# Kernel optimization log

Hardware: AMD Instinct MI355X
Metric: run time of the kernel (lower is better)

The kernel has to match this reference:

```python
import jax, jax.numpy as jnp
import numpy as np

N_NODES = 50000
N_EDGES = 800000
N_GRAPHS = 500
D_IN, D_HID, D_OUT = 128, 128, 64


def setup_inputs() -> dict:
    key = jax.random.key(0)
    ks = jax.random.split(key, 8)
    n_feat = jax.random.normal(ks[0], (N_NODES, D_IN), jnp.float32)
    src = jax.random.randint(ks[1], (N_EDGES,), 0, N_NODES, jnp.int32)
    dst = jax.random.randint(ks[2], (N_EDGES,), 0, N_NODES, jnp.int32)
    graph_ids = jnp.sort(jax.random.randint(ks[3], (N_NODES,), 0, N_GRAPHS, jnp.int32))
    W0 = jax.random.normal(ks[4], (D_IN, D_HID), jnp.float32) * 0.05
    b0 = jnp.zeros((D_HID,), jnp.float32)
    W1 = jax.random.normal(ks[5], (D_HID, D_HID), jnp.float32) * 0.05
    b1 = jnp.zeros((D_HID,), jnp.float32)
    W2 = jax.random.normal(ks[6], (D_HID, D_OUT), jnp.float32) * 0.05
    b2 = jnp.zeros((D_OUT,), jnp.float32)
    return dict(n_feat=n_feat, W0=W0, b0=b0, W1=W1, b1=b1, W2=W2, b2=b2,
                src=src, dst=dst, graph_ids=graph_ids)


def _gcn_layer(h, W, b, src, dst, norm_out, norm_in):
    # DGL GraphConv, norm='both': D_out^{-1/2} gather, sum-aggregate at dst,
    # D_in^{-1/2}, then linear transform + bias.
    m = (h * norm_out[:, None])[src]                        # [E, d] gather
    agg = jax.ops.segment_sum(m, dst, num_segments=N_NODES)  # [N, d] scatter-add
    return (agg * norm_in[:, None]) @ W + b


def reference(n_feat, W0, b0, W1, b1, W2, b2, src, dst, graph_ids):
    ones_e = jnp.ones((N_EDGES,), jnp.float32)
    deg_out = jax.ops.segment_sum(ones_e, src, num_segments=N_NODES)
    deg_in = jax.ops.segment_sum(ones_e, dst, num_segments=N_NODES)
    norm_out = jnp.where(deg_out > 0, jax.lax.rsqrt(jnp.maximum(deg_out, 1.0)), 0.0)
    norm_in = jnp.where(deg_in > 0, jax.lax.rsqrt(jnp.maximum(deg_in, 1.0)), 0.0)

    h = jax.nn.relu(_gcn_layer(n_feat, W0, b0, src, dst, norm_out, norm_in))
    h = jax.nn.relu(_gcn_layer(h, W1, b1, src, dst, norm_out, norm_in))
    h = jax.nn.relu(_gcn_layer(h, W2, b2, src, dst, norm_out, norm_in))

    # dgl.mean_nodes: per-graph mean over nodes
    sums = jax.ops.segment_sum(h, graph_ids, num_segments=N_GRAPHS)   # [G, D_OUT]
    counts = jax.ops.segment_sum(jnp.ones((N_NODES,), jnp.float32), graph_ids,
                                 num_segments=N_GRAPHS)
    return sums / jnp.maximum(counts, 1.0)[:, None]
```

## Files before the change

kernel.cpp:

```cpp
#include <hip/hip_runtime.h>
#include <hip/hip_bf16.h>

#define NN 50000
#define NE 800000
#define NG 500

#define NR 8
#define NC 32
#define RNG (NN / NR)
#define CHE (NE / NC)
#define SCB 13

__device__ __forceinline__ unsigned f2bf(float f) {
    unsigned u = __float_as_uint(f);
    return (u + 0x7fffu + ((u >> 16) & 1u)) >> 16;
}
__device__ __forceinline__ float bf2f(unsigned u16) {
    return __uint_as_float(u16 << 16);
}

__global__ __launch_bounds__(256) void degree_lds_kernel(
        const int* __restrict__ src, const int* __restrict__ dst,
        int* __restrict__ pin, int* __restrict__ pout) {
    __shared__ int hin[RNG], hout[RNG];
    const int tid   = threadIdx.x;
    const int r     = blockIdx.x & (NR - 1);
    const int c     = blockIdx.x / NR;
    const int rbase = r * RNG;
    for (int i = tid; i < RNG; i += 256) { hin[i] = 0; hout[i] = 0; }
    __syncthreads();
    const int4* s4 = (const int4*)(src + c * CHE);
    const int4* d4 = (const int4*)(dst + c * CHE);
    for (int i = tid; i < CHE / 4; i += 256) {
        int4 s = s4[i];
        int4 d = d4[i];
        unsigned a;
        a = (unsigned)(d.x - rbase); if (a < RNG) atomicAdd(&hin[a], 1);
        a = (unsigned)(d.y - rbase); if (a < RNG) atomicAdd(&hin[a], 1);
        a = (unsigned)(d.z - rbase); if (a < RNG) atomicAdd(&hin[a], 1);
        a = (unsigned)(d.w - rbase); if (a < RNG) atomicAdd(&hin[a], 1);
        a = (unsigned)(s.x - rbase); if (a < RNG) atomicAdd(&hout[a], 1);
        a = (unsigned)(s.y - rbase); if (a < RNG) atomicAdd(&hout[a], 1);
        a = (unsigned)(s.z - rbase); if (a < RNG) atomicAdd(&hout[a], 1);
        a = (unsigned)(s.w - rbase); if (a < RNG) atomicAdd(&hout[a], 1);
    }
    __syncthreads();
    for (int i = tid; i < RNG; i += 256) {
        pin [c * NN + rbase + i] = hin[i];
        pout[c * NN + rbase + i] = hout[i];
    }
}

__global__ void reduce_norms_kernel(const int* __restrict__ pin, const int* __restrict__ pout,
                                    int* __restrict__ deg_in_tot,
                                    float* __restrict__ norm_in,
                                    float* __restrict__ norm_out, int n) {
    int i = blockIdx.x * blockDim.x + threadIdx.x;
    if (i >= n) return;
    int di = 0, dq = 0;
    #pragma unroll
    for (int c = 0; c < NC; c++) {
        di += pin [c * NN + i];
        dq += pout[c * NN + i];
    }
    deg_in_tot[i] = di;
    norm_in[i]  = di > 0 ? 1.0f / sqrtf((float)di) : 0.f;
    norm_out[i] = dq > 0 ? 1.0f / sqrtf((float)dq) : 0.f;
}

__global__ __launch_bounds__(1024) void scan_block_sums(
        const int* __restrict__ deg, int* __restrict__ bsum, int n) {
    __shared__ int wsum[16];
    const int tid = threadIdx.x, lane = tid & 63, wv = tid >> 6;
    const int i0 = blockIdx.x * 4096 + tid * 4;
    int s = 0;
    if (i0 + 3 < n) {
        int4 v = *(const int4*)(deg + i0);
        s = v.x + v.y + v.z + v.w;
    } else if (i0 < n) {
        s = deg[i0];
        if (i0 + 1 < n) s += deg[i0 + 1];
        if (i0 + 2 < n) s += deg[i0 + 2];
    }
    #pragma unroll
    for (int off = 32; off > 0; off >>= 1) s += __shfl_down(s, off);
    if (lane == 0) wsum[wv] = s;
    __syncthreads();
    if (wv == 0) {
        int t = (lane < 16) ? wsum[lane] : 0;
        #pragma unroll
        for (int off = 8; off > 0; off >>= 1) t += __shfl_down(t, off);
        if (lane == 0) bsum[blockIdx.x] = t;
    }
}

__global__ __launch_bounds__(1024) void scan_apply(
        const int* __restrict__ deg, const int* __restrict__ bsum,
        int* __restrict__ row_ptr, int n) {
    __shared__ int wsum[16];
    const int tid = threadIdx.x, lane = tid & 63, wv = tid >> 6;
    const int b = blockIdx.x;
    int base = 0;
    for (int j = 0; j < SCB; j++) base += (j < b) ? bsum[j] : 0;
    const int i0 = b * 4096 + tid * 4;
    int v0 = 0, v1 = 0, v2 = 0, v3 = 0;
    if (i0 + 3 < n) {
        int4 v = *(const int4*)(deg + i0);
        v0 = v.x; v1 = v.y; v2 = v.z; v3 = v.w;
    } else if (i0 < n) {
        v0 = deg[i0];
        if (i0 + 1 < n) v1 = deg[i0 + 1];
        if (i0 + 2 < n) v2 = deg[i0 + 2];
    }
    const int l0 = v0, l1 = l0 + v1, l2 = l1 + v2, l3 = l2 + v3;
    int x = l3;
    #pragma unroll
    for (int off = 1; off < 64; off <<= 1) {
        int y = __shfl_up(x, off);
        if (lane >= off) x += y;
    }
    if (lane == 63) wsum[wv] = x;
    __syncthreads();
    if (wv == 0) {
        int t = (lane < 16) ? wsum[lane] : 0;
        int s = t;
        #pragma unroll
        for (int off = 1; off < 16; off <<= 1) {
            int y = __shfl_up(s, off);
            if (lane >= off) s += y;
        }
        if (lane < 16) wsum[lane] = s - t;
    }
    __syncthreads();
    const int pre = base + wsum[wv] + (x - l3);
    if (b == 0 && tid == 0) row_ptr[0] = 0;
    if (i0 < n)     row_ptr[i0 + 1] = pre + l0;
    if (i0 + 1 < n) row_ptr[i0 + 2] = pre + l1;
    if (i0 + 2 < n) row_ptr[i0 + 3] = pre + l2;
    if (i0 + 3 < n) row_ptr[i0 + 4] = pre + l3;
}

__global__ void chunk_offsets_kernel(const int* __restrict__ pin,
                                     const int* __restrict__ row_ptr,
                                     int* __restrict__ pcur, int n) {
    int i = blockIdx.x * blockDim.x + threadIdx.x;
    if (i >= n) return;
    int off = row_ptr[i];
    #pragma unroll
    for (int c = 0; c < NC; c++) {
        pcur[c * NN + i] = off;
        off += pin[c * NN + i];
    }
}

__global__ __launch_bounds__(256) void place_lds_kernel(
        const int* __restrict__ src, const int* __restrict__ dst,
        const int* __restrict__ pcur, int* __restrict__ esrc) {
    __shared__ int lcur[RNG];
    const int tid   = threadIdx.x;
    const int r     = blockIdx.x & (NR - 1);
    const int c     = blockIdx.x / NR;
    const int rbase = r * RNG;
    for (int i = tid; i < RNG; i += 256) lcur[i] = pcur[c * NN + rbase + i];
    __syncthreads();
    const int4* s4 = (const int4*)(src + c * CHE);
    const int4* d4 = (const int4*)(dst + c * CHE);
    for (int i = tid; i < CHE / 4; i += 256) {
        int4 s = s4[i];
        int4 d = d4[i];
        unsigned a;
        a = (unsigned)(d.x - rbase); if (a < RNG) esrc[atomicAdd(&lcur[a], 1)] = s.x;
        a = (unsigned)(d.y - rbase); if (a < RNG) esrc[atomicAdd(&lcur[a], 1)] = s.y;
        a = (unsigned)(d.z - rbase); if (a < RNG) esrc[atomicAdd(&lcur[a], 1)] = s.z;
        a = (unsigned)(d.w - rbase); if (a < RNG) esrc[atomicAdd(&lcur[a], 1)] = s.w;
    }
}

template<int DO, int ROWS, bool A16>
__global__ __launch_bounds__(256) void gemm_reg_bf(
        const void* __restrict__ Av, const float* __restrict__ W,
        const float* __restrict__ norm, unsigned short* __restrict__ out, int nrows) {
    constexpr int DI  = 128;
    constexpr int KC  = 32;
    constexpr int CXN = DO / 8;
    constexpr int RYN = 256 / CXN;
    static_assert(ROWS == RYN * 8, "tile mismatch");
    __shared__ float At[KC][ROWS + 4];
    __shared__ float Wl[KC][DO + 4];

    const int tid  = threadIdx.x;
    const int cx   = tid % CXN;
    const int ry   = tid / CXN;
    const int row0 = blockIdx.x * ROWS;

    float acc[8][8] = {};

    for (int kc = 0; kc < DI; kc += KC) {
        __syncthreads();
        constexpr int AF4 = ROWS * KC / 4;
        #pragma unroll
        for (int i = tid; i < AF4; i += 256) {
            int r  = i >> 3;
            int kq = i & 7;
            int gr = row0 + r;
            float v0 = 0.f, v1 = 0.f, v2 = 0.f, v3 = 0.f;
            if (gr < nrows) {
                float s = norm[gr];
                if constexpr (A16) {
                    const unsigned short* A = (const unsigned short*)Av;
                    uint2 u = *(const uint2*)(A + (size_t)gr * DI + kc + kq * 4);
                    v0 = bf2f(u.x & 0xffffu) * s; v1 = bf2f(u.x >> 16) * s;
                    v2 = bf2f(u.y & 0xffffu) * s; v3 = bf2f(u.y >> 16) * s;
                } else {
                    const float* A = (const float*)Av;
                    float4 v = ((const float4*)(A + (size_t)gr * DI + kc))[kq];
                    v0 = v.x * s; v1 = v.y * s; v2 = v.z * s; v3 = v.w * s;
                }
            }
            At[kq * 4 + 0][r] = v0;
            At[kq * 4 + 1][r] = v1;
            At[kq * 4 + 2][r] = v2;
            At[kq * 4 + 3][r] = v3;
        }
        constexpr int WF4 = KC * DO / 4;
        #pragma unroll
        for (int i = tid; i < WF4; i += 256) {
            int k  = i / (DO / 4);
            int c4 = i % (DO / 4);
            *(float4*)&Wl[k][c4 * 4] = ((const float4*)(W + (size_t)(kc + k) * DO))[c4];
        }
        __syncthreads();
        #pragma unroll 4
        for (int k = 0; k < KC; k++) {
            float a[8], w[8];
            *(float4*)&a[0] = *(const float4*)&At[k][ry * 4];
            *(float4*)&a[4] = *(const float4*)&At[k][ROWS / 2 + ry * 4];
            *(float4*)&w[0] = *(const float4*)&Wl[k][cx * 4];
            *(float4*)&w[4] = *(const float4*)&Wl[k][DO / 2 + cx * 4];
            #pragma unroll
            for (int i = 0; i < 8; i++)
                #pragma unroll
                for (int j = 0; j < 8; j++)
                    acc[i][j] += a[i] * w[j];
        }
    }
    #pragma unroll
    for (int i = 0; i < 8; i++) {
        int r  = (i < 4) ? (ry * 4 + i) : (ROWS / 2 + ry * 4 + (i - 4));
        int gr = row0 + r;
        if (gr < nrows) {
            unsigned short* orow = out + (size_t)gr * DO;
            uint2 lo, hi;
            lo.x = f2bf(acc[i][0]) | (f2bf(acc[i][1]) << 16);
            lo.y = f2bf(acc[i][2]) | (f2bf(acc[i][3]) << 16);
            hi.x = f2bf(acc[i][4]) | (f2bf(acc[i][5]) << 16);
            hi.y = f2bf(acc[i][6]) | (f2bf(acc[i][7]) << 16);
            ((uint2*)orow)[cx]            = lo;
            ((uint2*)(orow + DO / 2))[cx] = hi;
        }
    }
}

__global__ __launch_bounds__(256) void aggregate128_h16(
        const unsigned short* __restrict__ t, const int* __restrict__ row_ptr,
        const int* __restrict__ esrc, const float* __restrict__ norm_in,
        const float* __restrict__ bias, unsigned short* __restrict__ out, int n) {
    const int wid  = (blockIdx.x * blockDim.x + threadIdx.x) >> 6;
    const int lane = threadIdx.x & 63;
    if (wid >= n) return;
    const int beg = row_ptr[wid], end = row_ptr[wid + 1];
    const unsigned* tp = (const unsigned*)t;
    float ax0 = 0, ay0 = 0, ax1 = 0, ay1 = 0, ax2 = 0, ay2 = 0, ax3 = 0, ay3 = 0;
    int e = beg;
    for (; e + 3 < end; e += 4) {
        int s0 = esrc[e], s1 = esrc[e + 1], s2 = esrc[e + 2], s3 = esrc[e + 3];
        unsigned v0 = tp[(size_t)s0 * 64 + lane];
        unsigned v1 = tp[(size_t)s1 * 64 + lane];
        unsigned v2 = tp[(size_t)s2 * 64 + lane];
        unsigned v3 = tp[(size_t)s3 * 64 + lane];
        ax0 += bf2f(v0 & 0xffffu); ay0 += bf2f(v0 >> 16);
        ax1 += bf2f(v1 & 0xffffu); ay1 += bf2f(v1 >> 16);
        ax2 += bf2f(v2 & 0xffffu); ay2 += bf2f(v2 >> 16);
        ax3 += bf2f(v3 & 0xffffu); ay3 += bf2f(v3 >> 16);
    }
    for (; e < end; e++) {
        unsigned v = tp[(size_t)esrc[e] * 64 + lane];
        ax0 += bf2f(v & 0xffffu); ay0 += bf2f(v >> 16);
    }
    float ni = norm_in[wid];
    float2 bb = ((const float2*)bias)[lane];
    float ox = fmaxf((ax0 + ax1 + ax2 + ax3) * ni + bb.x, 0.f);
    float oy = fmaxf((ay0 + ay1 + ay2 + ay3) * ni + bb.y, 0.f);
    ((unsigned*)out)[(size_t)wid * 64 + lane] = f2bf(ox) | (f2bf(oy) << 16);
}

__global__ __launch_bounds__(256) void aggregate64_f32(
        const unsigned short* __restrict__ t, const int* __restrict__ row_ptr,
        const int* __restrict__ esrc, const float* __restrict__ norm_in,
        const float* __restrict__ bias, float* __restrict__ out, int n) {
    const int wid  = (blockIdx.x * blockDim.x + threadIdx.x) >> 6;
    const int lane = threadIdx.x & 63;
    if (wid >= n) return;
    const int beg = row_ptr[wid], end = row_ptr[wid + 1];
    float a0 = 0, a1 = 0, a2 = 0, a3 = 0;
    int e = beg;
    for (; e + 3 < end; e += 4) {
        int s0 = esrc[e], s1 = esrc[e + 1], s2 = esrc[e + 2], s3 = esrc[e + 3];
        a0 += bf2f(t[(size_t)s0 * 64 + lane]);
        a1 += bf2f(t[(size_t)s1 * 64 + lane]);
        a2 += bf2f(t[(size_t)s2 * 64 + lane]);
        a3 += bf2f(t[(size_t)s3 * 64 + lane]);
    }
    for (; e < end; e++) a0 += bf2f(t[(size_t)esrc[e] * 64 + lane]);
    float o = fmaxf((a0 + a1 + a2 + a3) * norm_in[wid] + bias[lane], 0.f);
    out[(size_t)wid * 64 + lane] = o;
}

__global__ __launch_bounds__(256) void readout_partial(
        const float* __restrict__ h, const int* __restrict__ gids,
        float* __restrict__ sums, float* __restrict__ counts, int n) {
    const int wid  = (blockIdx.x * blockDim.x + threadIdx.x) >> 6;
    const int lane = threadIdx.x & 63;
    const int beg = wid * 64;
    if (beg >= n) return;
    const int end = min(beg + 64, n);
    int cur = gids[beg];
    float acc = 0.f; int cnt = 0;
    for (int i = beg; i < end; i++) {
        int g = gids[i];
        if (g != cur) {
            atomicAdd(&sums[(size_t)cur * 64 + lane], acc);
            if (lane == 0) atomicAdd(&counts[cur], (float)cnt);
            cur = g; acc = 0.f; cnt = 0;
        }
        acc += h[(size_t)i * 64 + lane];
        cnt++;
    }
    atomicAdd(&sums[(size_t)cur * 64 + lane], acc);
    if (lane == 0) atomicAdd(&counts[cur], (float)cnt);
}

__global__ void finalize_kernel(const float* __restrict__ sums, const float* __restrict__ counts,
                                float* __restrict__ out, int total) {
    int i = blockIdx.x * blockDim.x + threadIdx.x;
    if (i < total) out[i] = sums[i] / fmaxf(counts[i >> 6], 1.f);
}

extern "C" void kernel_launch(void* const* d_in, const int* in_sizes, int n_in,
                              void* d_out, int out_size, void* d_ws, size_t ws_size,
                              hipStream_t stream) {
    const float* n_feat = (const float*)d_in[0];
    const float* W0 = (const float*)d_in[1];
    const float* b0 = (const float*)d_in[2];
    const float* W1 = (const float*)d_in[3];
    const float* b1 = (const float*)d_in[4];
    const float* W2 = (const float*)d_in[5];
    const float* b2 = (const float*)d_in[6];
    const int* src  = (const int*)d_in[7];
    const int* dst  = (const int*)d_in[8];
    const int* gids = (const int*)d_in[9];
    float* out = (float*)d_out;

    char* ws = (char*)d_ws;
    int*            esrc       = (int*)   (ws + 0);
    float*          norm_out   = (float*) (ws + 3200000);
    float*          norm_in    = (float*) (ws + 3400000);
    int*            deg_in_tot = (int*)   (ws + 3600000);
    int*            row_ptr    = (int*)   (ws + 3800000);
    int*            bsum       = (int*)   (ws + 4000064);
    float*          sums       = (float*) (ws + 4200064);
    float*          counts     = (float*) (ws + 4328064);
    unsigned short* bufA       = (unsigned short*)(ws + 4330112);
    int*            pin        = (int*)   (ws + 4330112);
    int*            pout       = (int*)   (ws + 4330112 + 6400000);
    int*            pcur       = (int*)   (ws + 17200000);
    unsigned short* bufB16     = (unsigned short*)(ws + 29930112);
    float*          bufBf      = (float*) (ws + 29930112);

    hipMemsetAsync(sums, 0, (NG * 64 + NG) * sizeof(float), stream);

    degree_lds_kernel<<<NR * NC, 256, 0, stream>>>(src, dst, pin, pout);
    reduce_norms_kernel<<<(NN + 255) / 256, 256, 0, stream>>>(pin, pout, deg_in_tot,
                                                              norm_in, norm_out, NN);
    scan_block_sums<<<SCB, 1024, 0, stream>>>(deg_in_tot, bsum, NN);
    scan_apply<<<SCB, 1024, 0, stream>>>(deg_in_tot, bsum, row_ptr, NN);
    chunk_offsets_kernel<<<(NN + 255) / 256, 256, 0, stream>>>(pin, row_ptr, pcur, NN);
    place_lds_kernel<<<NR * NC, 256, 0, stream>>>(src, dst, pcur, esrc);

    const int g128 = (NN + 127) / 128;
    const int g64  = (NN + 255) / 256;
    const int agg_grid = (NN + 3) / 4;

    gemm_reg_bf<128, 128, false><<<g128, 256, 0, stream>>>(n_feat, W0, norm_out, bufA, NN);
    aggregate128_h16<<<agg_grid, 256, 0, stream>>>(bufA, row_ptr, esrc, norm_in, b0, bufB16, NN);
    gemm_reg_bf<128, 128, true><<<g128, 256, 0, stream>>>(bufB16, W1, norm_out, bufA, NN);
    aggregate128_h16<<<agg_grid, 256, 0, stream>>>(bufA, row_ptr, esrc, norm_in, b1, bufB16, NN);
    gemm_reg_bf<64, 256, true><<<g64, 256, 0, stream>>>(bufB16, W2, norm_out, bufA, NN);
    aggregate64_f32<<<agg_grid, 256, 0, stream>>>(bufA, row_ptr, esrc, norm_in, b2, bufBf, NN);

    const int ro_threads = ((NN + 63) / 64) * 64;
    readout_partial<<<(ro_threads + 255) / 256, 256, 0, stream>>>(bufBf, gids, sums, counts, NN);
    finalize_kernel<<<(NG * 64 + 255) / 256, 256, 0, stream>>>(sums, counts, out, NG * 64);
}
```

Before: 377.2 us.

## Fuse block-sum scan into degree reduction and deepen gather unrolling to 8

```diff
diff --git a/kernel.cpp b/kernel.cpp
--- a/kernel.cpp
+++ b/kernel.cpp
@@ -21,12 +21,13 @@
 
 __global__ __launch_bounds__(256) void degree_lds_kernel(
         const int* __restrict__ src, const int* __restrict__ dst,
-        int* __restrict__ pin, int* __restrict__ pout) {
+        int* __restrict__ pin, int* __restrict__ pout, int* __restrict__ bsum) {
     __shared__ int hin[RNG], hout[RNG];
     const int tid   = threadIdx.x;
     const int r     = blockIdx.x & (NR - 1);
     const int c     = blockIdx.x / NR;
     const int rbase = r * RNG;
+    if (blockIdx.x == 0 && tid < SCB) bsum[tid] = 0;
     for (int i = tid; i < RNG; i += 256) { hin[i] = 0; hout[i] = 0; }
     __syncthreads();
     const int4* s4 = (const int4*)(src + c * CHE);
@@ -51,46 +52,35 @@
     }
 }
 
-__global__ void reduce_norms_kernel(const int* __restrict__ pin, const int* __restrict__ pout,
-                                    int* __restrict__ deg_in_tot,
-                                    float* __restrict__ norm_in,
-                                    float* __restrict__ norm_out, int n) {
-    int i = blockIdx.x * blockDim.x + threadIdx.x;
-    if (i >= n) return;
+__global__ __launch_bounds__(256) void reduce_norms_kernel(
+        const int* __restrict__ pin, const int* __restrict__ pout,
+        int* __restrict__ deg_in_tot, float* __restrict__ norm_in,
+        float* __restrict__ norm_out, int* __restrict__ bsum,
+        float* __restrict__ sums, int n) {
+    const int tid = threadIdx.x, lane = tid & 63, wv = tid >> 6;
+    const int i = blockIdx.x * 256 + tid;
+    const int gi = i;
+    if (gi < NG * 64 + NG) sums[gi] = 0.f;
     int di = 0, dq = 0;
-    #pragma unroll
-    for (int c = 0; c < NC; c++) {
-        di += pin [c * NN + i];
-        dq += pout[c * NN + i];
-    }
-    deg_in_tot[i] = di;
-    norm_in[i]  = di > 0 ? 1.0f / sqrtf((float)di) : 0.f;
-    norm_out[i] = dq > 0 ? 1.0f / sqrtf((float)dq) : 0.f;
-}
-
-__global__ __launch_bounds__(1024) void scan_block_sums(
-        const int* __restrict__ deg, int* __restrict__ bsum, int n) {
-    __shared__ int wsum[16];
-    const int tid = threadIdx.x, lane = tid & 63, wv = tid >> 6;
-    const int i0 = blockIdx.x * 4096 + tid * 4;
-    int s = 0;
-    if (i0 + 3 < n) {
-        int4 v = *(const int4*)(deg + i0);
-        s = v.x + v.y + v.z + v.w;
-    } else if (i0 < n) {
-        s = deg[i0];
-        if (i0 + 1 < n) s += deg[i0 + 1];
-        if (i0 + 2 < n) s += deg[i0 + 2];
-    }
+    if (i < n) {
+        #pragma unroll
+        for (int c = 0; c < NC; c++) {
+            di += pin [c * NN + i];
+            dq += pout[c * NN + i];
+        }
+        deg_in_tot[i] = di;
+        norm_in[i]  = di > 0 ? 1.0f / sqrtf((float)di) : 0.f;
+        norm_out[i] = dq > 0 ? 1.0f / sqrtf((float)dq) : 0.f;
+    }
+    __shared__ int wsum[4];
+    int s = di;
     #pragma unroll
     for (int off = 32; off > 0; off >>= 1) s += __shfl_down(s, off);
     if (lane == 0) wsum[wv] = s;
     __syncthreads();
-    if (wv == 0) {
-        int t = (lane < 16) ? wsum[lane] : 0;
-        #pragma unroll
-        for (int off = 8; off > 0; off >>= 1) t += __shfl_down(t, off);
-        if (lane == 0) bsum[blockIdx.x] = t;
+    if (tid == 0) {
+        int t = wsum[0] + wsum[1] + wsum[2] + wsum[3];
+        atomicAdd(&bsum[blockIdx.x >> 4], t);
     }
 }
 
@@ -270,27 +260,45 @@
     if (wid >= n) return;
     const int beg = row_ptr[wid], end = row_ptr[wid + 1];
     const unsigned* tp = (const unsigned*)t;
-    float ax0 = 0, ay0 = 0, ax1 = 0, ay1 = 0, ax2 = 0, ay2 = 0, ax3 = 0, ay3 = 0;
+    float ax[8] = {0, 0, 0, 0, 0, 0, 0, 0};
+    float ay[8] = {0, 0, 0, 0, 0, 0, 0, 0};
     int e = beg;
+    for (; e + 7 < end; e += 8) {
+        int sx[8];
+        #pragma unroll
+        for (int j = 0; j < 8; j++) sx[j] = esrc[e + j];
+        unsigned v[8];
+        #pragma unroll
+        for (int j = 0; j < 8; j++) v[j] = tp[(size_t)sx[j] * 64 + lane];
+        #pragma unroll
+        for (int j = 0; j < 8; j++) {
+            ax[j] += bf2f(v[j] & 0xffffu);
+            ay[j] += bf2f(v[j] >> 16);
+        }
+    }
     for (; e + 3 < end; e += 4) {
-        int s0 = esrc[e], s1 = esrc[e + 1], s2 = esrc[e + 2], s3 = esrc[e + 3];
-        unsigned v0 = tp[(size_t)s0 * 64 + lane];
-        unsigned v1 = tp[(size_t)s1 * 64 + lane];
-        unsigned v2 = tp[(size_t)s2 * 64 + lane];
-        unsigned v3 = tp[(size_t)s3 * 64 + lane];
-        ax0 += bf2f(v0 & 0xffffu); ay0 += bf2f(v0 >> 16);
-        ax1 += bf2f(v1 & 0xffffu); ay1 += bf2f(v1 >> 16);
-        ax2 += bf2f(v2 & 0xffffu); ay2 += bf2f(v2 >> 16);
-        ax3 += bf2f(v3 & 0xffffu); ay3 += bf2f(v3 >> 16);
+        int sx[4];
+        #pragma unroll
+        for (int j = 0; j < 4; j++) sx[j] = esrc[e + j];
+        unsigned v[4];
+        #pragma unroll
+        for (int j = 0; j < 4; j++) v[j] = tp[(size_t)sx[j] * 64 + lane];
+        #pragma unroll
+        for (int j = 0; j < 4; j++) {
+            ax[j] += bf2f(v[j] & 0xffffu);
+            ay[j] += bf2f(v[j] >> 16);
+        }
     }
     for (; e < end; e++) {
         unsigned v = tp[(size_t)esrc[e] * 64 + lane];
-        ax0 += bf2f(v & 0xffffu); ay0 += bf2f(v >> 16);
-    }
+        ax[0] += bf2f(v & 0xffffu); ay[0] += bf2f(v >> 16);
+    }
+    float sxx = ((ax[0] + ax[1]) + (ax[2] + ax[3])) + ((ax[4] + ax[5]) + (ax[6] + ax[7]));
+    float syy = ((ay[0] + ay[1]) + (ay[2] + ay[3])) + ((ay[4] + ay[5]) + (ay[6] + ay[7]));
     float ni = norm_in[wid];
     float2 bb = ((const float2*)bias)[lane];
-    float ox = fmaxf((ax0 + ax1 + ax2 + ax3) * ni + bb.x, 0.f);
-    float oy = fmaxf((ay0 + ay1 + ay2 + ay3) * ni + bb.y, 0.f);
+    float ox = fmaxf(sxx * ni + bb.x, 0.f);
+    float oy = fmaxf(syy * ni + bb.y, 0.f);
     ((unsigned*)out)[(size_t)wid * 64 + lane] = f2bf(ox) | (f2bf(oy) << 16);
 }
 
@@ -302,17 +310,31 @@
     const int lane = threadIdx.x & 63;
     if (wid >= n) return;
     const int beg = row_ptr[wid], end = row_ptr[wid + 1];
-    float a0 = 0, a1 = 0, a2 = 0, a3 = 0;
+    float a[8] = {0, 0, 0, 0, 0, 0, 0, 0};
     int e = beg;
+    for (; e + 7 < end; e += 8) {
+        int sx[8];
+        #pragma unroll
+        for (int j = 0; j < 8; j++) sx[j] = esrc[e + j];
+        unsigned short v[8];
+        #pragma unroll
+        for (int j = 0; j < 8; j++) v[j] = t[(size_t)sx[j] * 64 + lane];
+        #pragma unroll
+        for (int j = 0; j < 8; j++) a[j] += bf2f(v[j]);
+    }
     for (; e + 3 < end; e += 4) {
-        int s0 = esrc[e], s1 = esrc[e + 1], s2 = esrc[e + 2], s3 = esrc[e + 3];
-        a0 += bf2f(t[(size_t)s0 * 64 + lane]);
-        a1 += bf2f(t[(size_t)s1 * 64 + lane]);
-        a2 += bf2f(t[(size_t)s2 * 64 + lane]);
-        a3 += bf2f(t[(size_t)s3 * 64 + lane]);
-    }
-    for (; e < end; e++) a0 += bf2f(t[(size_t)esrc[e] * 64 + lane]);
-    float o = fmaxf((a0 + a1 + a2 + a3) * norm_in[wid] + bias[lane], 0.f);
+        int sx[4];
+        #pragma unroll
+        for (int j = 0; j < 4; j++) sx[j] = esrc[e + j];
+        unsigned short v[4];
+        #pragma unroll
+        for (int j = 0; j < 4; j++) v[j] = t[(size_t)sx[j] * 64 + lane];
+        #pragma unroll
+        for (int j = 0; j < 4; j++) a[j] += bf2f(v[j]);
+    }
+    for (; e < end; e++) a[0] += bf2f(t[(size_t)esrc[e] * 64 + lane]);
+    float s = ((a[0] + a[1]) + (a[2] + a[3])) + ((a[4] + a[5]) + (a[6] + a[7]));
+    float o = fmaxf(s * norm_in[wid] + bias[lane], 0.f);
     out[(size_t)wid * 64 + lane] = o;
 }
 
@@ -377,12 +399,10 @@
     unsigned short* bufB16     = (unsigned short*)(ws + 29930112);
     float*          bufBf      = (float*) (ws + 29930112);
 
-    hipMemsetAsync(sums, 0, (NG * 64 + NG) * sizeof(float), stream);
-
-    degree_lds_kernel<<<NR * NC, 256, 0, stream>>>(src, dst, pin, pout);
+    degree_lds_kernel<<<NR * NC, 256, 0, stream>>>(src, dst, pin, pout, bsum);
     reduce_norms_kernel<<<(NN + 255) / 256, 256, 0, stream>>>(pin, pout, deg_in_tot,
-                                                              norm_in, norm_out, NN);
-    scan_block_sums<<<SCB, 1024, 0, stream>>>(deg_in_tot, bsum, NN);
+                                                              norm_in, norm_out, bsum,
+                                                              sums, NN);
     scan_apply<<<SCB, 1024, 0, stream>>>(deg_in_tot, bsum, row_ptr, NN);
     chunk_offsets_kernel<<<(NN + 255) / 256, 256, 0, stream>>>(pin, row_ptr, pcur, NN);
     place_lds_kernel<<<NR * NC, 256, 0, stream>>>(src, dst, pcur, esrc);
```

After: 359.0 us. 4.8% less time.
